# Performance work log

Hardware: AMD Instinct MI355X
Metric: run time of the kernel (lower is better)

## Reference

```python
import jax, jax.numpy as jnp
import numpy as np

# Grid / problem constants
D = H = W_SP = 128      # spatial_shape of the sparse tensor (single batch)
N = 200_000             # number of active voxels
C = 64                  # nchan
K = 5                   # SubMConv3d kernel_size
PAD = 2                 # padding (stride=1 submanifold => output sites == input sites)
EPS = 1e-5              # BatchNorm eps (torch default)


def setup_inputs() -> dict:
    key = jax.random.key(0)
    k1, k2, k3 = jax.random.split(key, 3)
    # unique active voxel coordinates: permute linear grid indices, take first N
    lin = jax.random.permutation(k1, D * H * W_SP)[:N]
    z = lin // (H * W_SP)
    y = (lin // W_SP) % H
    x = lin % W_SP
    coords = jnp.stack([z, y, x], axis=1).astype(jnp.int32)   # [N,3]
    feats = jax.random.normal(k2, (N, C), jnp.float32)        # [N,C]
    std = (2.0 / (K ** 3 * C)) ** 0.5
    Wt = jax.random.normal(k3, (K ** 3, C, C), jnp.float32) * std  # [125,Cin,Cout]
    bias = jnp.full((C,), -0.01, jnp.float32)
    gamma = jnp.ones((C,), jnp.float32)   # bn weight (init 1)
    beta = jnp.zeros((C,), jnp.float32)   # bn bias (init 0)
    return {"feats": feats, "coords": coords, "Wt": Wt, "bias": bias,
            "gamma": gamma, "beta": beta}


def _subm_conv(feats, coords, Wt, bias):
    """Submanifold sparse 3D conv: out[p] = sum_k W_k @ feat[p + off_k], active only."""
    lin = (coords[:, 0] * H + coords[:, 1]) * W_SP + coords[:, 2]
    # dense hash: grid position -> active-voxel row index (or -1)
    idx_map = jnp.full((D * H * W_SP,), -1, jnp.int32).at[lin].set(
        jnp.arange(N, dtype=jnp.int32))
    r = jnp.arange(-PAD, PAD + 1)
    offs = jnp.stack(jnp.meshgrid(r, r, r, indexing="ij"), axis=-1)
    offs = offs.reshape(-1, 3).astype(jnp.int32)              # [125,3]
    bounds = jnp.array([D, H, W_SP], jnp.int32)

    def step(acc, kw):
        Wk, off = kw                                          # [C,C], [3]
        nb = coords + off                                     # [N,3]
        valid = jnp.all((nb >= 0) & (nb < bounds), axis=1)    # [N]
        nlin = (nb[:, 0] * H + nb[:, 1]) * W_SP + nb[:, 2]
        j = idx_map[jnp.where(valid, nlin, 0)]                # [N]
        ok = valid & (j >= 0)
        f = jnp.where(ok[:, None], feats[jnp.maximum(j, 0)], 0.0)  # gather [N,C]
        return acc + f @ Wk, None

    acc0 = jnp.zeros((N, C), feats.dtype)
    out, _ = jax.lax.scan(step, acc0, (Wt, offs))
    return out + bias


def reference(feats, coords, Wt, bias, gamma, beta):
    h = _subm_conv(feats, coords, Wt, bias)
    # BatchNorm1d over active voxels (training-mode batch statistics)
    mean = h.mean(axis=0)
    var = ((h - mean) ** 2).mean(axis=0)
    h = (h - mean) * jax.lax.rsqrt(var + EPS) * gamma + beta
    return jax.nn.elu(h)
```

## Files before the change

kernel.cpp:

```cpp
#include <hip/hip_runtime.h>
#include <hip/hip_bf16.h>

#define NVOX 200000
#define NK   125
#define GRID_LIN (128 * 128 * 128)

#define WT_OFF    0u
#define STATS_OFF 1024000u
#define PFX_OFF   1024512u
#define OLD_OFF   1032704u
#define FB_OFF    1832704u
#define IDX_OFF   27432832u

#define F16N   (NVOX * 16)
#define WCONV_N (NK * 4096)
#define PREP_N (F16N + 16 + WCONV_N)

typedef short bf16x8 __attribute__((ext_vector_type(8)));
typedef float f32x4  __attribute__((ext_vector_type(4)));
typedef unsigned short u16x4 __attribute__((ext_vector_type(4)));
typedef unsigned int uint_as1 __attribute__((address_space(1)));
typedef unsigned int uint_as3 __attribute__((address_space(3)));

static __device__ __forceinline__ unsigned short f2bf(float f) {
    union { float f; unsigned int u; } v; v.f = f;
    unsigned int u = v.u;
    return (unsigned short)((u + 0x7FFFu + ((u >> 16) & 1u)) >> 16);
}

__global__ __launch_bounds__(256) void scatter_kernel(const int* __restrict__ coords,
                                                      int* __restrict__ idx_map) {
    int p = blockIdx.x * 256 + threadIdx.x;
    if (p < NVOX) {
        int z = coords[p * 3 + 0], y = coords[p * 3 + 1], x = coords[p * 3 + 2];
        idx_map[(z << 14) | (y << 7) | x] = p;
    }
}

__global__ __launch_bounds__(1024) void count_kernel(const int* __restrict__ idx_map,
                                                     int* __restrict__ pfx) {
    __shared__ int wsum[16];
    int i = blockIdx.x * 1024 + threadIdx.x;
    int bit = idx_map[i] >= 0 ? 1 : 0;
    unsigned long long m = __ballot(bit);
    int lane = threadIdx.x & 63, wave = threadIdx.x >> 6;
    if (lane == 0) wsum[wave] = __popcll(m);
    __syncthreads();
    if (threadIdx.x == 0) {
        int s = 0;
#pragma unroll
        for (int w = 0; w < 16; ++w) s += wsum[w];
        pfx[blockIdx.x] = s;
    }
}

__global__ __launch_bounds__(1024) void scan_kernel(int* __restrict__ pfx) {
    __shared__ int A[2048], B[2048];
    int t = threadIdx.x;
    A[t] = pfx[t]; A[t + 1024] = pfx[t + 1024];
    __syncthreads();
    int* src = A; int* dst = B;
    for (int off = 1; off < 2048; off <<= 1) {
        dst[t]        = src[t]        + (t >= off ? src[t - off] : 0);
        dst[t + 1024] = src[t + 1024] + src[t + 1024 - off];
        __syncthreads();
        int* tmp = src; src = dst; dst = tmp;
    }
    pfx[t]        = t ? src[t - 1] : 0;
    pfx[t + 1024] = src[t + 1023];
}

__global__ __launch_bounds__(1024) void relabel_kernel(const int* __restrict__ pfx,
                                                       int* __restrict__ idx_map,
                                                       int* __restrict__ oldof) {
    __shared__ int wsum[16];
    int i = blockIdx.x * 1024 + threadIdx.x;
    int old = idx_map[i];
    int bit = old >= 0 ? 1 : 0;
    unsigned long long m = __ballot(bit);
    int lane = threadIdx.x & 63, wave = threadIdx.x >> 6;
    int intra = __popcll(m & ((1ull << lane) - 1ull));
    if (lane == 0) wsum[wave] = __popcll(m);
    __syncthreads();
    int woff = 0;
    for (int w = 0; w < wave; ++w) woff += wsum[w];
    if (bit) {
        int nid = pfx[blockIdx.x] + woff + intra;
        idx_map[i] = nid;
        oldof[nid] = old;
    }
}

__global__ __launch_bounds__(256) void prep_kernel(const float* __restrict__ Wt,
                                                   const float* __restrict__ feats,
                                                   const int* __restrict__ oldof,
                                                   unsigned short* __restrict__ wt,
                                                   unsigned short* __restrict__ fb) {
    int i = blockIdx.x * 256 + threadIdx.x;
    if (i < F16N) {
        int p = i >> 4, c = i & 15;
        int old = oldof[p];
        f32x4 f = *(const f32x4*)(feats + (size_t)old * 64 + c * 4);
        u16x4 u;
        u[0] = f2bf(f[0]); u[1] = f2bf(f[1]); u[2] = f2bf(f[2]); u[3] = f2bf(f[3]);
        *(u16x4*)(fb + (size_t)i * 4) = u;
    } else if (i < F16N + 16) {
        *(u16x4*)(fb + (size_t)i * 4) = (u16x4)0;
    } else if (i < PREP_N) {
        int j = i - (F16N + 16);
        int k = j >> 12, r = j & 4095;
        int a2h = r >> 9;
        int ln  = (r >> 3) & 63;
        int e   = r & 7;
        int co  = (a2h >> 1) * 16 + (ln & 15);
        int ci  = (a2h & 1) * 32 + ((ln >> 4) << 3) + e;
        wt[(k << 12) + r] = f2bf(Wt[(k << 12) + (ci << 6) + co]);
    }
}

#define PROBEG(ge_, jj_) do {                                                \
    int dz_ = (ge_) / 5 - 2, dy_ = (ge_) % 5 - 2;                            \
    int nz_ = z + dz_, ny_ = y + dy_;                                        \
    bool rok_ = live && ((unsigned)nz_ < 128u) && ((unsigned)ny_ < 128u);    \
    int base_ = (nz_ << 14) | (ny_ << 7);                                    \
    _Pragma("unroll")                                                        \
    for (int kk_ = 0; kk_ < 5; ++kk_) {                                      \
        int nx_ = x + kk_ - 2;                                               \
        jj_[kk_] = (rok_ && ((unsigned)nx_ < 128u)) ? idx_map[base_ | nx_]   \
                                                    : -1;                    \
    }                                                                        \
} while (0)

#define STAGE(j5v, slot_) do {                                               \
    unsigned short* dst_ = &lds_b[wave][slot_][lane * 8];                    \
    _Pragma("unroll")                                                        \
    for (int i_ = 0; i_ < 8; ++i_) {                                         \
        int jv_ = __shfl((j5v), i_ * 8 + (lane >> 3), 64);                   \
        const char* src_ = fbp + ((size_t)(unsigned)jv_ << 7) + coff;        \
        __builtin_amdgcn_global_load_lds((const uint_as1*)(const void*)src_, \
            (uint_as3*)(void*)(dst_ + i_ * 512), 16, 0, 0);                  \
    }                                                                        \
} while (0)

#define KK(kk_, slot_) do {                                                  \
    asm volatile("s_waitcnt vmcnt(8)" ::: "memory");                         \
    __builtin_amdgcn_sched_barrier(0);                                       \
    const char* bs_ = bwave + (slot_) * 8192;                                \
    bf16x8 b0_[4], b1_[4];                                                   \
    _Pragma("unroll")                                                        \
    for (int t_ = 0; t_ < 4; ++t_) {                                         \
        b0_[t_] = *(const bf16x8*)(bs_ + t_ * 2048 + sw0);                   \
        b1_[t_] = *(const bf16x8*)(bs_ + t_ * 2048 + sw1);                   \
    }                                                                        \
    __builtin_amdgcn_sched_barrier(0);                                       \
    const char* wk_ = wk + (size_t)(kk_) * 8192;                             \
    bf16x8 af0_[4], af1_[4];                                                 \
    _Pragma("unroll")                                                        \
    for (int a_ = 0; a_ < 4; ++a_) {                                         \
        af0_[a_] = *(const bf16x8*)(wk_ + a_ * 2048);                        \
        af1_[a_] = *(const bf16x8*)(wk_ + a_ * 2048 + 1024);                 \
    }                                                                        \
    if ((kk_) + 2 < 5) STAGE(j5[(kk_) + 2], (kk_) & 1);                      \
    _Pragma("unroll")                                                        \
    for (int t_ = 0; t_ < 4; ++t_) {                                         \
        if ((unsigned)((mk[kk_] >> (t_ * 16)) & 0xFFFFull)) {                \
            _Pragma("unroll")                                                \
            for (int a_ = 0; a_ < 4; ++a_) {                                 \
                acc[a_][t_] = __builtin_amdgcn_mfma_f32_16x16x32_bf16(       \
                    af0_[a_], b0_[t_], acc[a_][t_], 0, 0, 0);                \
                acc[a_][t_] = __builtin_amdgcn_mfma_f32_16x16x32_bf16(       \
                    af1_[a_], b1_[t_], acc[a_][t_], 0, 0, 0);                \
            }                                                                \
        }                                                                    \
    }                                                                        \
} while (0)

__global__ __launch_bounds__(256, 2) void conv_kernel(
    const int* __restrict__ coords, const unsigned short* __restrict__ fb,
    const unsigned short* __restrict__ wt, const int* __restrict__ idx_map,
    const int* __restrict__ oldof,
    float* __restrict__ out, float* __restrict__ stats) {
    __shared__ unsigned short lds_b[4][2][4096];

    const int vblk = (blockIdx.x & 7) * 98 + (blockIdx.x >> 3);
    const int vbase = vblk * 256;
    if (vbase >= NVOX) return;

    const int tid  = threadIdx.x;
    const int wave = tid >> 6;
    const int lane = tid & 63;
    const int g    = lane >> 4;
    const int l15  = lane & 15;
    const int vox  = vbase + tid;
    const bool live = vox < NVOX;
    const int rot  = vblk % 25;

    int z = 0, y = 0, x = 0;
    if (live) {
        int old = oldof[vox];
        z = coords[old * 3 + 0]; y = coords[old * 3 + 1]; x = coords[old * 3 + 2];
    }

    const int coff = (((lane & 7) ^ ((lane >> 3) & 7)) << 4);
    const int sw0  = ((g    ) ^ (l15 & 7)) << 4;
    const int sw1  = ((4 + g) ^ (l15 & 7)) << 4;
    const char* bwave = (const char*)&lds_b[wave][0][0] + (l15 << 7);
    const char* fbp = (const char*)fb;
    const char* wtp = (const char*)wt + lane * 16;

    f32x4 acc[4][4];
#pragma unroll
    for (int a = 0; a < 4; ++a)
#pragma unroll
        for (int b = 0; b < 4; ++b) acc[a][b] = (f32x4)0.0f;

    int j5[5];
    unsigned long long mk[5];
    {
        int jj[5];
        PROBEG(rot, jj);
#pragma unroll
        for (int kk = 0; kk < 5; ++kk) {
            mk[kk] = __ballot(jj[kk] >= 0);
            j5[kk] = jj[kk] < 0 ? NVOX : jj[kk];
        }
    }

#pragma unroll 1
    for (int grp = 0; grp < 25; ++grp) {
        int ge = grp + rot; if (ge >= 25) ge -= 25;
        const char* wk = wtp + (size_t)(ge * 5) * 8192;

        STAGE(j5[0], 0);
        STAGE(j5[1], 1);

        int jn[5];
        if (grp < 24) {
            int ge2 = ge + 1; if (ge2 >= 25) ge2 -= 25;
            PROBEG(ge2, jn);
        }

        KK(0, 0); KK(1, 1); KK(2, 0); KK(3, 1); KK(4, 0);

        if (grp < 24) {
#pragma unroll
            for (int kk = 0; kk < 5; ++kk) {
                mk[kk] = __ballot(jn[kk] >= 0);
                j5[kk] = jn[kk] < 0 ? NVOX : jn[kk];
            }
        }
        __syncthreads();
    }

#pragma unroll
    for (int b = 0; b < 4; ++b) {
        int v = vbase + wave * 64 + b * 16 + l15;
        if (v < NVOX) {
            int o = oldof[v];
#pragma unroll
            for (int a = 0; a < 4; ++a)
                *(f32x4*)(out + (size_t)o * 64 + a * 16 + g * 4) = acc[a][b];
        }
    }

    float s1[16], s2[16];
#pragma unroll
    for (int a = 0; a < 4; ++a)
#pragma unroll
        for (int r = 0; r < 4; ++r) {
            float s = 0.f, q = 0.f;
#pragma unroll
            for (int b = 0; b < 4; ++b) { float xv = acc[a][b][r]; s += xv; q += xv * xv; }
            s1[a * 4 + r] = s; s2[a * 4 + r] = q;
        }
#pragma unroll
    for (int m = 1; m < 16; m <<= 1) {
#pragma unroll
        for (int i = 0; i < 16; ++i) {
            s1[i] += __shfl_xor(s1[i], m, 64);
            s2[i] += __shfl_xor(s2[i], m, 64);
        }
    }
    if (l15 == 0) {
#pragma unroll
        for (int a = 0; a < 4; ++a)
#pragma unroll
            for (int r = 0; r < 4; ++r) {
                int co = a * 16 + g * 4 + r;
                atomicAdd(&stats[co],      s1[a * 4 + r]);
                atomicAdd(&stats[64 + co], s2[a * 4 + r]);
            }
    }
}

__global__ __launch_bounds__(256) void finalize_kernel(float* __restrict__ out,
                                                       const float* __restrict__ stats,
                                                       const float* __restrict__ gamma,
                                                       const float* __restrict__ beta) {
    int i = blockIdx.x * 256 + threadIdx.x;
    if (i >= NVOX * 16) return;
    int cg = (i & 15) * 4;
    f32x4 v = *(f32x4*)(out + (size_t)i * 4);
    f32x4 r;
#pragma unroll
    for (int c = 0; c < 4; ++c) {
        int co = cg + c;
        float mean = stats[co] * (1.0f / NVOX);
        float var  = stats[64 + co] * (1.0f / NVOX) - mean * mean;
        float sc   = rsqrtf(var + 1e-5f) * gamma[co];
        float sh   = beta[co] - mean * sc;
        float yv   = v[c] * sc + sh;
        r[c] = yv > 0.f ? yv : expm1f(yv);
    }
    *(f32x4*)(out + (size_t)i * 4) = r;
}

extern "C" void kernel_launch(void* const* d_in, const int* in_sizes, int n_in,
                              void* d_out, int out_size, void* d_ws, size_t ws_size,
                              hipStream_t stream) {
    const float* feats  = (const float*)d_in[0];
    const int*   coords = (const int*)d_in[1];
    const float* Wt     = (const float*)d_in[2];
    const float* gamma  = (const float*)d_in[4];
    const float* beta   = (const float*)d_in[5];
    float* out = (float*)d_out;
    char*  ws  = (char*)d_ws;

    unsigned short* wt  = (unsigned short*)(ws + WT_OFF);
    float* stats        = (float*)(ws + STATS_OFF);
    int*   pfx          = (int*)(ws + PFX_OFF);
    int*   oldof        = (int*)(ws + OLD_OFF);
    unsigned short* fb  = (unsigned short*)(ws + FB_OFF);
    int*   idx_map      = (int*)(ws + IDX_OFF);

    hipMemsetAsync(idx_map, 0xFF, (size_t)GRID_LIN * 4, stream);
    hipMemsetAsync(stats, 0, 128 * 4, stream);

    scatter_kernel<<<(NVOX + 255) / 256, 256, 0, stream>>>(coords, idx_map);
    count_kernel<<<GRID_LIN / 1024, 1024, 0, stream>>>(idx_map, pfx);
    scan_kernel<<<1, 1024, 0, stream>>>(pfx);
    relabel_kernel<<<GRID_LIN / 1024, 1024, 0, stream>>>(pfx, idx_map, oldof);
    prep_kernel<<<(PREP_N + 255) / 256, 256, 0, stream>>>(Wt, feats, oldof, wt, fb);
    conv_kernel<<<784, 256, 0, stream>>>(coords, fb, wt, idx_map, oldof, out, stats);
    finalize_kernel<<<12500, 256, 0, stream>>>(out, stats, gamma, beta);
}
```

Baseline: 680.6 us.

## Split conv work across 8 waves of 32 voxels each with tuned waitcnts

Each conv block now runs 512 threads (8 waves), and each wave covers 32 voxels instead of 64. This halves per-wave accumulators and LDS staging, with the goal of more waves in flight to hide gather latency. The change also makes the neighbor probe branchless with a clamped address, always prefetches the next group, sets explicit per-step vmcnt waits, and raises MFMA priority with s_setprio. It risks extra weight-fragment loads per voxel, since each wave now reloads the same A fragments for half as many voxels, and it depends on the hand-tuned waitcnt values being correct.

Result: slower. 1.034 ms (+52.0%).

```diff
diff --git a/kernel.cpp b/kernel.cpp
--- a/kernel.cpp
+++ b/kernel.cpp
@@ -121,20 +121,22 @@
 #define PROBEG(ge_, jj_) do {                                                \
     int dz_ = (ge_) / 5 - 2, dy_ = (ge_) % 5 - 2;                            \
     int nz_ = z + dz_, ny_ = y + dy_;                                        \
-    bool rok_ = live && ((unsigned)nz_ < 128u) && ((unsigned)ny_ < 128u);    \
+    bool rok_ = plive && ((unsigned)nz_ < 128u) && ((unsigned)ny_ < 128u);   \
     int base_ = (nz_ << 14) | (ny_ << 7);                                    \
     _Pragma("unroll")                                                        \
     for (int kk_ = 0; kk_ < 5; ++kk_) {                                      \
         int nx_ = x + kk_ - 2;                                               \
-        jj_[kk_] = (rok_ && ((unsigned)nx_ < 128u)) ? idx_map[base_ | nx_]   \
-                                                    : -1;                    \
+        bool ok_ = rok_ && ((unsigned)nx_ < 128u);                           \
+        int addr_ = ok_ ? (base_ | nx_) : 0;                                 \
+        int t_ = idx_map[addr_];                                             \
+        jj_[kk_] = ok_ ? t_ : -1;                                            \
     }                                                                        \
 } while (0)
 
 #define STAGE(j5v, slot_) do {                                               \
-    unsigned short* dst_ = &lds_b[wave][slot_][lane * 8];                    \
+    unsigned short* dst_ = &lds_b[wave][slot_][0] + lane * 8;                \
     _Pragma("unroll")                                                        \
-    for (int i_ = 0; i_ < 8; ++i_) {                                         \
+    for (int i_ = 0; i_ < 4; ++i_) {                                         \
         int jv_ = __shfl((j5v), i_ * 8 + (lane >> 3), 64);                   \
         const char* src_ = fbp + ((size_t)(unsigned)jv_ << 7) + coff;        \
         __builtin_amdgcn_global_load_lds((const uint_as1*)(const void*)src_, \
@@ -142,16 +144,14 @@
     }                                                                        \
 } while (0)
 
-#define KK(kk_, slot_) do {                                                  \
-    asm volatile("s_waitcnt vmcnt(8)" ::: "memory");                         \
+#define KK(kk_, slot_, VM_) do {                                             \
+    asm volatile("s_waitcnt vmcnt(" #VM_ ")" ::: "memory");                  \
     __builtin_amdgcn_sched_barrier(0);                                       \
-    const char* bs_ = bwave + (slot_) * 8192;                                \
-    bf16x8 b0_[4], b1_[4];                                                   \
-    _Pragma("unroll")                                                        \
-    for (int t_ = 0; t_ < 4; ++t_) {                                         \
-        b0_[t_] = *(const bf16x8*)(bs_ + t_ * 2048 + sw0);                   \
-        b1_[t_] = *(const bf16x8*)(bs_ + t_ * 2048 + sw1);                   \
-    }                                                                        \
+    const char* bs_ = bwave + (slot_) * 4096;                                \
+    bf16x8 b0A_ = *(const bf16x8*)(bs_ + sw0);                               \
+    bf16x8 b1A_ = *(const bf16x8*)(bs_ + sw1);                               \
+    bf16x8 b0B_ = *(const bf16x8*)(bs_ + 2048 + sw0);                        \
+    bf16x8 b1B_ = *(const bf16x8*)(bs_ + 2048 + sw1);                        \
     __builtin_amdgcn_sched_barrier(0);                                       \
     const char* wk_ = wk + (size_t)(kk_) * 8192;                             \
     bf16x8 af0_[4], af1_[4];                                                 \
@@ -160,27 +160,39 @@
         af0_[a_] = *(const bf16x8*)(wk_ + a_ * 2048);                        \
         af1_[a_] = *(const bf16x8*)(wk_ + a_ * 2048 + 1024);                 \
     }                                                                        \
+    __builtin_amdgcn_sched_barrier(0);                                       \
     if ((kk_) + 2 < 5) STAGE(j5[(kk_) + 2], (kk_) & 1);                      \
-    _Pragma("unroll")                                                        \
-    for (int t_ = 0; t_ < 4; ++t_) {                                         \
-        if ((unsigned)((mk[kk_] >> (t_ * 16)) & 0xFFFFull)) {                \
-            _Pragma("unroll")                                                \
-            for (int a_ = 0; a_ < 4; ++a_) {                                 \
-                acc[a_][t_] = __builtin_amdgcn_mfma_f32_16x16x32_bf16(       \
-                    af0_[a_], b0_[t_], acc[a_][t_], 0, 0, 0);                \
-                acc[a_][t_] = __builtin_amdgcn_mfma_f32_16x16x32_bf16(       \
-                    af1_[a_], b1_[t_], acc[a_][t_], 0, 0, 0);                \
-            }                                                                \
+    __builtin_amdgcn_sched_barrier(0);                                       \
+    __builtin_amdgcn_s_setprio(1);                                           \
+    unsigned mA_ = (unsigned)(mk[kk_] & 0xFFFFull);                          \
+    unsigned mB_ = (unsigned)((mk[kk_] >> 16) & 0xFFFFull);                  \
+    if (mA_) {                                                               \
+        _Pragma("unroll")                                                    \
+        for (int a_ = 0; a_ < 4; ++a_) {                                     \
+            accA[a_] = __builtin_amdgcn_mfma_f32_16x16x32_bf16(              \
+                af0_[a_], b0A_, accA[a_], 0, 0, 0);                          \
+            accA[a_] = __builtin_amdgcn_mfma_f32_16x16x32_bf16(              \
+                af1_[a_], b1A_, accA[a_], 0, 0, 0);                          \
         }                                                                    \
     }                                                                        \
+    if (mB_) {                                                               \
+        _Pragma("unroll")                                                    \
+        for (int a_ = 0; a_ < 4; ++a_) {                                     \
+            accB[a_] = __builtin_amdgcn_mfma_f32_16x16x32_bf16(              \
+                af0_[a_], b0B_, accB[a_], 0, 0, 0);                          \
+            accB[a_] = __builtin_amdgcn_mfma_f32_16x16x32_bf16(              \
+                af1_[a_], b1B_, accB[a_], 0, 0, 0);                          \
+        }                                                                    \
+    }                                                                        \
+    __builtin_amdgcn_s_setprio(0);                                           \
 } while (0)
 
-__global__ __launch_bounds__(256, 2) void conv_kernel(
+__global__ __launch_bounds__(512, 4) void conv_kernel(
     const int* __restrict__ coords, const unsigned short* __restrict__ fb,
     const unsigned short* __restrict__ wt, const int* __restrict__ idx_map,
     const int* __restrict__ oldof,
     float* __restrict__ out, float* __restrict__ stats) {
-    __shared__ unsigned short lds_b[4][2][4096];
+    __shared__ unsigned short lds_b[8][2][2048];
 
     const int vblk = (blockIdx.x & 7) * 98 + (blockIdx.x >> 3);
     const int vbase = vblk * 256;
@@ -191,13 +203,15 @@
     const int lane = tid & 63;
     const int g    = lane >> 4;
     const int l15  = lane & 15;
-    const int vox  = vbase + tid;
-    const bool live = vox < NVOX;
     const int rot  = vblk % 25;
 
+    const int wvox = vbase + wave * 32;
+    const int pv   = wvox + (lane & 31);
+    const bool plive = pv < NVOX;
+
     int z = 0, y = 0, x = 0;
-    if (live) {
-        int old = oldof[vox];
+    if (plive) {
+        int old = oldof[pv];
         z = coords[old * 3 + 0]; y = coords[old * 3 + 1]; x = coords[old * 3 + 2];
     }
 
@@ -208,11 +222,9 @@
     const char* fbp = (const char*)fb;
     const char* wtp = (const char*)wt + lane * 16;
 
-    f32x4 acc[4][4];
-#pragma unroll
-    for (int a = 0; a < 4; ++a)
-#pragma unroll
-        for (int b = 0; b < 4; ++b) acc[a][b] = (f32x4)0.0f;
+    f32x4 accA[4], accB[4];
+#pragma unroll
+    for (int a = 0; a < 4; ++a) { accA[a] = (f32x4)0.0f; accB[a] = (f32x4)0.0f; }
 
     int j5[5];
     unsigned long long mk[5];
@@ -235,12 +247,11 @@
         STAGE(j5[1], 1);
 
         int jn[5];
-        if (grp < 24) {
-            int ge2 = ge + 1; if (ge2 >= 25) ge2 -= 25;
-            PROBEG(ge2, jn);
-        }
-
-        KK(0, 0); KK(1, 1); KK(2, 0); KK(3, 1); KK(4, 0);
+        int ge2 = ge + 1; if (ge2 >= 25) ge2 -= 25;
+        PROBEG(ge2, jn);
+        __builtin_amdgcn_sched_barrier(0);
+
+        KK(0, 0, 9); KK(1, 1, 17); KK(2, 0, 12); KK(3, 1, 12); KK(4, 0, 8);
 
         if (grp < 24) {
 #pragma unroll
@@ -252,14 +263,20 @@
         __syncthreads();
     }
 
-#pragma unroll
-    for (int b = 0; b < 4; ++b) {
-        int v = vbase + wave * 64 + b * 16 + l15;
-        if (v < NVOX) {
-            int o = oldof[v];
+    {
+        int vA = wvox + l15;
+        if (vA < NVOX) {
+            int o = oldof[vA];
 #pragma unroll
             for (int a = 0; a < 4; ++a)
-                *(f32x4*)(out + (size_t)o * 64 + a * 16 + g * 4) = acc[a][b];
+                *(f32x4*)(out + (size_t)o * 64 + a * 16 + g * 4) = accA[a];
+        }
+        int vB = wvox + 16 + l15;
+        if (vB < NVOX) {
+            int o = oldof[vB];
+#pragma unroll
+            for (int a = 0; a < 4; ++a)
+                *(f32x4*)(out + (size_t)o * 64 + a * 16 + g * 4) = accB[a];
         }
     }
 
@@ -268,10 +285,9 @@
     for (int a = 0; a < 4; ++a)
 #pragma unroll
         for (int r = 0; r < 4; ++r) {
-            float s = 0.f, q = 0.f;
-#pragma unroll
-            for (int b = 0; b < 4; ++b) { float xv = acc[a][b][r]; s += xv; q += xv * xv; }
-            s1[a * 4 + r] = s; s2[a * 4 + r] = q;
+            float xa = accA[a][r], xb = accB[a][r];
+            s1[a * 4 + r] = xa + xb;
+            s2[a * 4 + r] = xa * xa + xb * xb;
         }
 #pragma unroll
     for (int m = 1; m < 16; m <<= 1) {
@@ -341,6 +357,6 @@
     scan_kernel<<<1, 1024, 0, stream>>>(pfx);
     relabel_kernel<<<GRID_LIN / 1024, 1024, 0, stream>>>(pfx, idx_map, oldof);
     prep_kernel<<<(PREP_N + 255) / 256, 256, 0, stream>>>(Wt, feats, oldof, wt, fb);
-    conv_kernel<<<784, 256, 0, stream>>>(coords, fb, wt, idx_map, oldof, out, stats);
+    conv_kernel<<<784, 512, 0, stream>>>(coords, fb, wt, idx_map, oldof, out, stats);
     finalize_kernel<<<12500, 256, 0, stream>>>(out, stats, gamma, beta);
 }
```

## Stage weights in LDS via triple buffer and load neighbor features directly to registers

Applied to the files above, without the earlier changes.

Gathered neighbor features were staged into per-wave LDS. They are now loaded straight from global memory into MFMA B-operand registers. The per-offset weight tiles are instead staged block-wide into a three-slot LDS ring with async global-to-LDS loads, a swizzled layout from the prep kernel, and s_barrier handshakes. Occupancy is raised to 3 blocks per SM, MFMA sections get elevated priority, and the idx_map probe is made branchless. The trade-off is one barrier per kernel offset plus uncoalesced 16-byte register gathers, in exchange for sharing weight loads across the four waves and using less LDS.

Result: slower. 754.8 us (+10.9%).

```diff
diff --git a/kernel.cpp b/kernel.cpp
--- a/kernel.cpp
+++ b/kernel.cpp
@@ -109,12 +109,9 @@
     } else if (i < PREP_N) {
         int j = i - (F16N + 16);
         int k = j >> 12, r = j & 4095;
-        int a2h = r >> 9;
-        int ln  = (r >> 3) & 63;
-        int e   = r & 7;
-        int co  = (a2h >> 1) * 16 + (ln & 15);
-        int ci  = (a2h & 1) * 32 + ((ln >> 4) << 3) + e;
-        wt[(k << 12) + r] = f2bf(Wt[(k << 12) + (ci << 6) + co]);
+        int co = r >> 6, ci = r & 63;
+        int dst = (co << 6) | ((((ci >> 3) ^ (co & 7)) << 3) | (ci & 7));
+        wt[(k << 12) + dst] = f2bf(Wt[(k << 12) + (ci << 6) + co]);
     }
 }
 
@@ -126,41 +123,47 @@
     _Pragma("unroll")                                                        \
     for (int kk_ = 0; kk_ < 5; ++kk_) {                                      \
         int nx_ = x + kk_ - 2;                                               \
-        jj_[kk_] = (rok_ && ((unsigned)nx_ < 128u)) ? idx_map[base_ | nx_]   \
-                                                    : -1;                    \
+        bool ok_ = rok_ && ((unsigned)nx_ < 128u);                           \
+        int addr_ = ok_ ? (base_ | nx_) : 0;                                 \
+        int t_ = idx_map[addr_];                                             \
+        jj_[kk_] = ok_ ? t_ : -1;                                            \
     }                                                                        \
 } while (0)
 
-#define STAGE(j5v, slot_) do {                                               \
-    unsigned short* dst_ = &lds_b[wave][slot_][lane * 8];                    \
-    _Pragma("unroll")                                                        \
-    for (int i_ = 0; i_ < 8; ++i_) {                                         \
-        int jv_ = __shfl((j5v), i_ * 8 + (lane >> 3), 64);                   \
-        const char* src_ = fbp + ((size_t)(unsigned)jv_ << 7) + coff;        \
-        __builtin_amdgcn_global_load_lds((const uint_as1*)(const void*)src_, \
-            (uint_as3*)(void*)(dst_ + i_ * 512), 16, 0, 0);                  \
-    }                                                                        \
+#define STAGEW(k_, sl_) do {                                                 \
+    const unsigned short* s_ = wt + ((size_t)(unsigned)(k_) << 12) + tid * 8;\
+    unsigned short* d_ = lds_w + (sl_) * 4096 + tid * 8;                     \
+    __builtin_amdgcn_global_load_lds((const uint_as1*)(const void*)s_,       \
+        (uint_as3*)(void*)d_, 16, 0, 0);                                     \
+    __builtin_amdgcn_global_load_lds((const uint_as1*)(const void*)(s_+2048),\
+        (uint_as3*)(void*)(d_ + 2048), 16, 0, 0);                            \
 } while (0)
 
-#define KK(kk_, slot_) do {                                                  \
-    asm volatile("s_waitcnt vmcnt(8)" ::: "memory");                         \
-    __builtin_amdgcn_sched_barrier(0);                                       \
-    const char* bs_ = bwave + (slot_) * 8192;                                \
+#define KK(kk_, VM_, stk_) do {                                              \
     bf16x8 b0_[4], b1_[4];                                                   \
     _Pragma("unroll")                                                        \
     for (int t_ = 0; t_ < 4; ++t_) {                                         \
-        b0_[t_] = *(const bf16x8*)(bs_ + t_ * 2048 + sw0);                   \
-        b1_[t_] = *(const bf16x8*)(bs_ + t_ * 2048 + sw1);                   \
+        int jv_ = __shfl(j5[kk_], t_ * 16 + l15, 64);                        \
+        const char* rp_ = fbp + ((size_t)(unsigned)jv_ << 7) + (g << 4);     \
+        b0_[t_] = *(const bf16x8*)(rp_);                                     \
+        b1_[t_] = *(const bf16x8*)(rp_ + 64);                                \
     }                                                                        \
+    asm volatile("s_waitcnt vmcnt(" #VM_ ")" ::: "memory");                  \
+    __builtin_amdgcn_s_barrier();                                            \
     __builtin_amdgcn_sched_barrier(0);                                       \
-    const char* wk_ = wk + (size_t)(kk_) * 8192;                             \
+    int rs_ = s0 + (kk_); if (rs_ >= 3) rs_ -= 3; if (rs_ >= 3) rs_ -= 3;    \
+    const char* wb_ = (const char*)(lds_w + rs_ * 4096);                     \
     bf16x8 af0_[4], af1_[4];                                                 \
     _Pragma("unroll")                                                        \
     for (int a_ = 0; a_ < 4; ++a_) {                                         \
-        af0_[a_] = *(const bf16x8*)(wk_ + a_ * 2048);                        \
-        af1_[a_] = *(const bf16x8*)(wk_ + a_ * 2048 + 1024);                 \
+        af0_[a_] = *(const bf16x8*)(wb_ + (((a_ * 16 + l15) << 7) | sw0));   \
+        af1_[a_] = *(const bf16x8*)(wb_ + (((a_ * 16 + l15) << 7) | sw1));   \
     }                                                                        \
-    if ((kk_) + 2 < 5) STAGE(j5[(kk_) + 2], (kk_) & 1);                      \
+    __builtin_amdgcn_sched_barrier(0);                                       \
+    int st_ = rs_ + 2; if (st_ >= 3) st_ -= 3;                               \
+    STAGEW((stk_), st_);                                                     \
+    __builtin_amdgcn_sched_barrier(0);                                       \
+    __builtin_amdgcn_s_setprio(1);                                           \
     _Pragma("unroll")                                                        \
     for (int t_ = 0; t_ < 4; ++t_) {                                         \
         if ((unsigned)((mk[kk_] >> (t_ * 16)) & 0xFFFFull)) {                \
@@ -173,14 +176,15 @@
             }                                                                \
         }                                                                    \
     }                                                                        \
+    __builtin_amdgcn_s_setprio(0);                                           \
 } while (0)
 
-__global__ __launch_bounds__(256, 2) void conv_kernel(
+__global__ __launch_bounds__(256, 3) void conv_kernel(
     const int* __restrict__ coords, const unsigned short* __restrict__ fb,
     const unsigned short* __restrict__ wt, const int* __restrict__ idx_map,
     const int* __restrict__ oldof,
     float* __restrict__ out, float* __restrict__ stats) {
-    __shared__ unsigned short lds_b[4][2][4096];
+    __shared__ __align__(16) unsigned short lds_w[3 * 4096];
 
     const int vblk = (blockIdx.x & 7) * 98 + (blockIdx.x >> 3);
     const int vbase = vblk * 256;
@@ -200,19 +204,16 @@
         int old = oldof[vox];
         z = coords[old * 3 + 0]; y = coords[old * 3 + 1]; x = coords[old * 3 + 2];
     }
-
-    const int coff = (((lane & 7) ^ ((lane >> 3) & 7)) << 4);
-    const int sw0  = ((g    ) ^ (l15 & 7)) << 4;
-    const int sw1  = ((4 + g) ^ (l15 & 7)) << 4;
-    const char* bwave = (const char*)&lds_b[wave][0][0] + (l15 << 7);
+    const int sw0 = ((g    ) ^ (l15 & 7)) << 4;
+    const int sw1 = ((g + 4) ^ (l15 & 7)) << 4;
+
+    f32x4 acc[4][4];
+#pragma unroll
+    for (int a = 0; a < 4; ++a)
+#pragma unroll
+        for (int b = 0; b < 4; ++b) acc[a][b] = (f32x4)0.0f;
+
     const char* fbp = (const char*)fb;
-    const char* wtp = (const char*)wt + lane * 16;
-
-    f32x4 acc[4][4];
-#pragma unroll
-    for (int a = 0; a < 4; ++a)
-#pragma unroll
-        for (int b = 0; b < 4; ++b) acc[a][b] = (f32x4)0.0f;
 
     int j5[5];
     unsigned long long mk[5];
@@ -225,22 +226,26 @@
             j5[kk] = jj[kk] < 0 ? NVOX : jj[kk];
         }
     }
-
+    STAGEW(rot * 5 + 0, 0);
+    STAGEW(rot * 5 + 1, 1);
+
+    int s0 = 0;
 #pragma unroll 1
     for (int grp = 0; grp < 25; ++grp) {
         int ge = grp + rot; if (ge >= 25) ge -= 25;
-        const char* wk = wtp + (size_t)(ge * 5) * 8192;
-
-        STAGE(j5[0], 0);
-        STAGE(j5[1], 1);
+        int ge2 = ge + 1;  if (ge2 >= 25) ge2 -= 25;
+        const int kb = ge * 5;
+        const int nb = ge2 * 5;
 
         int jn[5];
-        if (grp < 24) {
-            int ge2 = ge + 1; if (ge2 >= 25) ge2 -= 25;
-            PROBEG(ge2, jn);
-        }
-
-        KK(0, 0); KK(1, 1); KK(2, 0); KK(3, 1); KK(4, 0);
+        PROBEG(ge2, jn);
+        __builtin_amdgcn_sched_barrier(0);
+
+        KK(0, 15, kb + 2);
+        KK(1, 23, kb + 3);
+        KK(2, 18, kb + 4);
+        KK(3, 18, nb + 0);
+        KK(4, 18, nb + 1);
 
         if (grp < 24) {
 #pragma unroll
@@ -249,8 +254,9 @@
                 j5[kk] = jn[kk] < 0 ? NVOX : jn[kk];
             }
         }
-        __syncthreads();
-    }
+        s0 += 2; if (s0 >= 3) s0 -= 3;
+    }
+    asm volatile("s_waitcnt vmcnt(0)" ::: "memory");
 
 #pragma unroll
     for (int b = 0; b < 4; ++b) {
```
